# Kernel optimization log

Hardware: AMD Instinct MI355X
Metric: run time of the kernel (lower is better)

Reference implementation:

```python
import jax, jax.numpy as jnp
import numpy as np

N_NODES = 50000
IN_DIM = 5000
OUT_DIM = 128
NNZ_X = 1000000
NNZ_ADJ = 1600000


def setup_inputs() -> dict:
    key = jax.random.key(0)
    k1, k2, k3, k4, k5, k6, k7 = jax.random.split(key, 7)
    x_rows = jax.random.randint(k1, (NNZ_X,), 0, N_NODES, dtype=jnp.int32)
    x_cols = jax.random.randint(k2, (NNZ_X,), 0, IN_DIM, dtype=jnp.int32)
    x_vals = jax.random.normal(k3, (NNZ_X,), dtype=jnp.float32)
    adj_rows = jax.random.randint(k4, (NNZ_ADJ,), 0, N_NODES, dtype=jnp.int32)
    adj_cols = jax.random.randint(k5, (NNZ_ADJ,), 0, N_NODES, dtype=jnp.int32)
    adj_vals = jax.random.uniform(k6, (NNZ_ADJ,), dtype=jnp.float32)
    # Glorot-uniform init as in weight_variable_glorot
    init_range = np.sqrt(6.0 / (IN_DIM + OUT_DIM))
    W = jax.random.uniform(k7, (IN_DIM, OUT_DIM), dtype=jnp.float32,
                           minval=-init_range, maxval=init_range)
    return {"x_rows": x_rows, "x_cols": x_cols, "x_vals": x_vals,
            "adj_rows": adj_rows, "adj_cols": adj_cols, "adj_vals": adj_vals,
            "W": W}


def reference(x_rows, x_cols, x_vals, adj_rows, adj_cols, adj_vals, W):
    # dropout = 0 -> sparse dropout is identity (keep_prob = 1).
    # Step 1: xw = sparse_x @ W  -> [N, D] via gather rows of W + segment sum over node ids
    xw = jax.ops.segment_sum(x_vals[:, None] * W[x_cols], x_rows,
                             num_segments=N_NODES)  # [N, D]
    # Step 2: out = sparse_adj @ xw  -> gather neighbor features, weight, scatter-add
    agg = jax.ops.segment_sum(adj_vals[:, None] * xw[adj_cols], adj_rows,
                              num_segments=N_NODES)  # [N, D]
    return jax.nn.relu(agg)
```

## Files before the change

kernel.cpp:

```cpp
#include <hip/hip_runtime.h>

#define ODIM 128
#define BROWS 128
#define NBMAX 512
#define TILE 4096
#define CMASK 0x1FFFFu
#define HISTB 1024
#define CONVB 512

typedef unsigned u32;
typedef unsigned long long u64;

__device__ inline unsigned f2bf(float x) {
  unsigned u = __float_as_uint(x);
  return (u + 0x7fffu + ((u >> 16) & 1u)) >> 16;
}


__global__ __launch_bounds__(256) void hist_conv(
    const int* __restrict__ xr, int nx, const int* __restrict__ ar, int na,
    int* __restrict__ ghX, int* __restrict__ ghA,
    const float2* __restrict__ W2, u32* __restrict__ Wbf, int wwords) {
  __shared__ int lh[2 * NBMAX];
  if ((int)blockIdx.x >= HISTB) {
    int i = (blockIdx.x - HISTB) * 256 + threadIdx.x;
    int stride = CONVB * 256;
    for (; i < wwords; i += stride) {
      float2 w = W2[i];
      Wbf[i] = f2bf(w.x) | (f2bf(w.y) << 16);
    }
    return;
  }
  for (int i = threadIdx.x; i < 2 * NBMAX; i += 256) lh[i] = 0;
  __syncthreads();
  int total = nx + na;
  for (int i = blockIdx.x * 256 + threadIdx.x; i < total; i += HISTB * 256) {
    if (i < nx) atomicAdd(&lh[xr[i] >> 7], 1);
    else        atomicAdd(&lh[NBMAX + (ar[i - nx] >> 7)], 1);
  }
  __syncthreads();
  for (int b = threadIdx.x; b < NBMAX; b += 256) {
    if (lh[b])         atomicAdd(&ghX[b], lh[b]);
    if (lh[NBMAX + b]) atomicAdd(&ghA[b], lh[NBMAX + b]);
  }
}


__global__ __launch_bounds__(NBMAX) void scan_buckets(
    int* __restrict__ ghX, int* __restrict__ baseX, int* __restrict__ curX,
    int* __restrict__ ghA, int* __restrict__ baseA, int* __restrict__ curA,
    int nb) {
  int* gh   = blockIdx.x ? ghA   : ghX;
  int* base = blockIdx.x ? baseA : baseX;
  int* cur  = blockIdx.x ? curA  : curX;
  __shared__ int s[NBMAX];
  int tid = threadIdx.x;
  int v = (tid < nb) ? gh[tid] : 0;
  s[tid] = v;
  __syncthreads();
  for (int off = 1; off < NBMAX; off <<= 1) {
    int t = (tid >= off) ? s[tid - off] : 0;
    __syncthreads();
    s[tid] += t;
    __syncthreads();
  }
  int excl = s[tid] - v;
  if (tid < nb) { base[tid] = excl; cur[tid] = excl; }
  if (tid == NBMAX - 1) base[nb] = s[tid];
}


__global__ __launch_bounds__(256) void partition_both(
    const int* __restrict__ xr, const int* __restrict__ xc,
    const float* __restrict__ xv, int nx, int ntX,
    int* __restrict__ curX, uint2* __restrict__ outX,
    const int* __restrict__ ar, const int* __restrict__ ac,
    const float* __restrict__ av, int na,
    int* __restrict__ curA, uint2* __restrict__ outA) {
  __shared__ uint2 pay[TILE];
  __shared__ unsigned short bkt[TILE];
  __shared__ unsigned short perm[TILE];
  __shared__ int hist[NBMAX];
  __shared__ int scn[NBMAX];
  __shared__ int cur[NBMAX];
  __shared__ int gbase[NBMAX];
  __shared__ int part[256];

  const int* rows; const int* cols; const float* vals;
  int nnz; int* gcur; uint2* outbuf; int tile;
  if ((int)blockIdx.x < ntX) {
    rows = xr; cols = xc; vals = xv; nnz = nx; gcur = curX; outbuf = outX;
    tile = blockIdx.x;
  } else {
    rows = ar; cols = ac; vals = av; nnz = na; gcur = curA; outbuf = outA;
    tile = blockIdx.x - ntX;
  }

  int tid = threadIdx.x;
  int tbase = tile * TILE;
  int cnt = nnz - tbase; if (cnt > TILE) cnt = TILE;

  for (int b = tid; b < NBMAX; b += 256) hist[b] = 0;
  __syncthreads();

  for (int j = tid; j < cnt; j += 256) {
    int r = rows[tbase + j];
    int c = cols[tbase + j];
    float v = vals[tbase + j];
    unsigned b = (unsigned)r >> 7;
    bkt[j] = (unsigned short)b;
    pay[j] = make_uint2(((unsigned)(r & 127) << 17) | (unsigned)c, __float_as_uint(v));
    atomicAdd(&hist[b], 1);
  }
  __syncthreads();

  int h0 = hist[2 * tid], h1 = hist[2 * tid + 1];
  int psum = h0 + h1;
  part[tid] = psum;
  __syncthreads();
  for (int off = 1; off < 256; off <<= 1) {
    int t = (tid >= off) ? part[tid - off] : 0;
    __syncthreads();
    part[tid] += t;
    __syncthreads();
  }
  int excl = part[tid] - psum;
  scn[2 * tid] = excl;     scn[2 * tid + 1] = excl + h0;
  cur[2 * tid] = excl;     cur[2 * tid + 1] = excl + h0;
  __syncthreads();

  for (int j = tid; j < cnt; j += 256) {
    int pos = atomicAdd(&cur[bkt[j]], 1);
    perm[pos] = (unsigned short)j;
  }
  for (int b = tid; b < NBMAX; b += 256) {
    int c = hist[b];
    if (c) gbase[b] = atomicAdd(&gcur[b], c);
  }
  __syncthreads();

  for (int p = tid; p < cnt; p += 256) {
    int j = perm[p];
    int b = bkt[j];
    outbuf[gbase[b] + (p - scn[b])] = pay[j];
  }
}


__global__ __launch_bounds__(256) void bucket_sort_both(
    int nbX,
    const int* __restrict__ baseX, const uint2* __restrict__ binX,
    uint2* __restrict__ boutX, int* __restrict__ rpX,
    const int* __restrict__ baseA, const uint2* __restrict__ binA,
    uint2* __restrict__ boutA, int* __restrict__ rpA, int N) {
  __shared__ int hist[BROWS], scn[BROWS], cur[BROWS];
  const int* base; const uint2* bufin; uint2* bufout; int* rowptr; int b;
  if ((int)blockIdx.x < nbX) {
    base = baseX; bufin = binX; bufout = boutX; rowptr = rpX; b = blockIdx.x;
  } else {
    base = baseA; bufin = binA; bufout = boutA; rowptr = rpA; b = blockIdx.x - nbX;
  }
  int tid = threadIdx.x;
  int e0 = base[b], ecnt = base[b + 1] - e0;

  if (tid < BROWS) hist[tid] = 0;
  __syncthreads();
  for (int j = tid; j < ecnt; j += 256)
    atomicAdd(&hist[bufin[e0 + j].x >> 17], 1);
  __syncthreads();

  int v = (tid < BROWS) ? hist[tid] : 0;
  if (tid < BROWS) scn[tid] = v;
  __syncthreads();
  for (int off = 1; off < BROWS; off <<= 1) {
    int t = (tid < BROWS && tid >= off) ? scn[tid - off] : 0;
    __syncthreads();
    if (tid < BROWS) scn[tid] += t;
    __syncthreads();
  }
  if (tid < BROWS) {
    int excl = scn[tid] - v;
    cur[tid] = excl;
    int node = b * BROWS + tid;
    if (node <= N) rowptr[node] = e0 + excl;
  }
  __syncthreads();

  for (int j = tid; j < ecnt; j += 256) {
    uint2 e = bufin[e0 + j];
    int pos = atomicAdd(&cur[e.x >> 17], 1);
    bufout[e0 + pos] = e;
  }
}


__global__ __launch_bounds__(256) void pull_x(
    const int* __restrict__ rowptr, const uint2* __restrict__ cv,
    const u32* __restrict__ Wbf, unsigned* __restrict__ xw, int nrows) {
  int lane = threadIdx.x & 63;
  int r = blockIdx.x * 4 + (threadIdx.x >> 6);
  if (r >= nrows) return;
  int e = rowptr[r], end = rowptr[r + 1];
  const u64* cv8 = (const u64*)cv;
  float acc0[8], acc1[8];
#pragma unroll
  for (int u = 0; u < 8; ++u) { acc0[u] = 0.f; acc1[u] = 0.f; }
  for (; e + 7 < end; e += 8) {
    u64 pk[8]; unsigned xg[8];
#pragma unroll
    for (int u = 0; u < 8; ++u) pk[u] = __builtin_nontemporal_load(cv8 + e + u);
#pragma unroll
    for (int u = 0; u < 8; ++u)
      xg[u] = Wbf[(size_t)((unsigned)pk[u] & CMASK) * 64 + lane];
#pragma unroll
    for (int u = 0; u < 8; ++u) {
      float v = __uint_as_float((unsigned)(pk[u] >> 32));
      acc0[u] += v * __uint_as_float(xg[u] << 16);
      acc1[u] += v * __uint_as_float(xg[u] & 0xffff0000u);
    }
  }
  for (; e < end; ++e) {
    u64 pk = __builtin_nontemporal_load(cv8 + e);
    unsigned ua = Wbf[(size_t)((unsigned)pk & CMASK) * 64 + lane];
    float va = __uint_as_float((unsigned)(pk >> 32));
    acc0[0] += va * __uint_as_float(ua << 16);
    acc1[0] += va * __uint_as_float(ua & 0xffff0000u);
  }
  float o0 = ((acc0[0] + acc0[1]) + (acc0[2] + acc0[3])) +
             ((acc0[4] + acc0[5]) + (acc0[6] + acc0[7]));
  float o1 = ((acc1[0] + acc1[1]) + (acc1[2] + acc1[3])) +
             ((acc1[4] + acc1[5]) + (acc1[6] + acc1[7]));
  xw[(size_t)r * 64 + lane] = f2bf(o0) | (f2bf(o1) << 16);
}

__global__ __launch_bounds__(256) void pull_a(
    const int* __restrict__ rowptr, const uint2* __restrict__ cv,
    const unsigned* __restrict__ xw, float2* __restrict__ out, int nrows) {
  int lane = threadIdx.x & 63;
  int r = blockIdx.x * 4 + (threadIdx.x >> 6);
  if (r >= nrows) return;
  int e = rowptr[r], end = rowptr[r + 1];
  const u64* cv8 = (const u64*)cv;
  float acc0[8], acc1[8];
#pragma unroll
  for (int u = 0; u < 8; ++u) { acc0[u] = 0.f; acc1[u] = 0.f; }
  for (; e + 7 < end; e += 8) {
    u64 pk[8]; unsigned xg[8];
#pragma unroll
    for (int u = 0; u < 8; ++u) pk[u] = __builtin_nontemporal_load(cv8 + e + u);
#pragma unroll
    for (int u = 0; u < 8; ++u)
      xg[u] = xw[(size_t)((unsigned)pk[u] & CMASK) * 64 + lane];
#pragma unroll
    for (int u = 0; u < 8; ++u) {
      float v = __uint_as_float((unsigned)(pk[u] >> 32));
      acc0[u] += v * __uint_as_float(xg[u] << 16);
      acc1[u] += v * __uint_as_float(xg[u] & 0xffff0000u);
    }
  }
  for (; e < end; ++e) {
    u64 pk = __builtin_nontemporal_load(cv8 + e);
    unsigned ua = xw[(size_t)((unsigned)pk & CMASK) * 64 + lane];
    float va = __uint_as_float((unsigned)(pk >> 32));
    acc0[0] += va * __uint_as_float(ua << 16);
    acc1[0] += va * __uint_as_float(ua & 0xffff0000u);
  }
  float o0 = ((acc0[0] + acc0[1]) + (acc0[2] + acc0[3])) +
             ((acc0[4] + acc0[5]) + (acc0[6] + acc0[7]));
  float o1 = ((acc1[0] + acc1[1]) + (acc1[2] + acc1[3])) +
             ((acc1[4] + acc1[5]) + (acc1[6] + acc1[7]));
  u64 ov = (u64)__float_as_uint(fmaxf(o0, 0.f)) |
           ((u64)__float_as_uint(fmaxf(o1, 0.f)) << 32);
  __builtin_nontemporal_store(ov, (u64*)(out + (size_t)r * 64 + lane));
}


__global__ __launch_bounds__(256) void spmm_scatter(
    const int* __restrict__ rows, const int* __restrict__ cols,
    const float* __restrict__ vals, const float* __restrict__ B,
    float* __restrict__ out, int nnz) {
  int e = blockIdx.x * 2 + (threadIdx.x >> 7);
  int d = threadIdx.x & (ODIM - 1);
  if (e >= nnz) return;
  atomicAdd(&out[(size_t)rows[e] * ODIM + d],
            vals[e] * B[(size_t)cols[e] * ODIM + d]);
}

__global__ __launch_bounds__(256) void relu_inplace(float* __restrict__ p, long n4) {
  long i = (long)blockIdx.x * blockDim.x + threadIdx.x;
  long stride = (long)gridDim.x * blockDim.x;
  float4* p4 = (float4*)p;
  for (long j = i; j < n4; j += stride) {
    float4 v = p4[j];
    v.x = fmaxf(v.x, 0.f); v.y = fmaxf(v.y, 0.f);
    v.z = fmaxf(v.z, 0.f); v.w = fmaxf(v.w, 0.f);
    p4[j] = v;
  }
}

extern "C" void kernel_launch(void* const* d_in, const int* in_sizes, int n_in,
                              void* d_out, int out_size, void* d_ws, size_t ws_size,
                              hipStream_t stream) {
  const int*   x_rows   = (const int*)d_in[0];
  const int*   x_cols   = (const int*)d_in[1];
  const float* x_vals   = (const float*)d_in[2];
  const int*   adj_rows = (const int*)d_in[3];
  const int*   adj_cols = (const int*)d_in[4];
  const float* adj_vals = (const float*)d_in[5];
  const float* W        = (const float*)d_in[6];

  const int nnz_x   = in_sizes[0];
  const int nnz_adj = in_sizes[3];
  const int wlen    = in_sizes[6];
  const int N       = out_size / ODIM;
  const int NB      = (N + BROWS - 1) / BROWS;
  const int ntX     = (nnz_x + TILE - 1) / TILE;
  const int ntA     = (nnz_adj + TILE - 1) / TILE;
  const int wwords  = wlen / 2;

  float* out = (float*)d_out;

  char* p = (char*)d_ws;
  int* ghX   = (int*)p;  p += NBMAX * sizeof(int);
  int* ghA   = (int*)p;  p += NBMAX * sizeof(int);
  int* baseX = (int*)p;  p += (NBMAX + 1) * sizeof(int);
  int* baseA = (int*)p;  p += (NBMAX + 1) * sizeof(int);
  int* curX  = (int*)p;  p += NBMAX * sizeof(int);
  int* curA  = (int*)p;  p += NBMAX * sizeof(int);
  int* rpX   = (int*)p;  p += (size_t)(N + 1) * sizeof(int);
  int* rpA   = (int*)p;  p += (size_t)(N + 1) * sizeof(int);
  p = (char*)(((uintptr_t)p + 255) & ~(uintptr_t)255);
  u32* Wbf   = (u32*)p;  p += (size_t)wwords * sizeof(u32);
  p = (char*)(((uintptr_t)p + 255) & ~(uintptr_t)255);
  char* bufs = p;

  const size_t xw_bytes = (size_t)N * 64 * sizeof(u32);

  {
    char* q = bufs;
    uint2* bufPX = (uint2*)q; q += (size_t)nnz_x * sizeof(uint2);
    uint2* bufPA = (uint2*)q; q += (size_t)nnz_adj * sizeof(uint2);
    uint2* bufSX = (uint2*)q; q += (size_t)nnz_x * sizeof(uint2);
    uint2* bufSA = (uint2*)q; q += (size_t)nnz_adj * sizeof(uint2);
    size_t need = (size_t)(q - (char*)d_ws);
    bool xw_fits = xw_bytes <= ((size_t)nnz_x + nnz_adj) * sizeof(uint2);
    if (ws_size >= need && NB <= NBMAX && xw_fits) {
      u32* xw = (u32*)bufPX;
      (void)hipMemsetAsync(ghX, 0, 2 * NBMAX * sizeof(int), stream);
      hist_conv<<<HISTB + CONVB, 256, 0, stream>>>(
          x_rows, nnz_x, adj_rows, nnz_adj, ghX, ghA,
          (const float2*)W, Wbf, wwords);
      scan_buckets<<<2, NBMAX, 0, stream>>>(ghX, baseX, curX, ghA, baseA, curA, NB);
      partition_both<<<ntX + ntA, 256, 0, stream>>>(
          x_rows, x_cols, x_vals, nnz_x, ntX, curX, bufPX,
          adj_rows, adj_cols, adj_vals, nnz_adj, curA, bufPA);
      bucket_sort_both<<<2 * NB, 256, 0, stream>>>(
          NB, baseX, bufPX, bufSX, rpX, baseA, bufPA, bufSA, rpA, N);
      pull_x<<<(N + 3) / 4, 256, 0, stream>>>(rpX, bufSX, Wbf, xw, N);
      pull_a<<<(N + 3) / 4, 256, 0, stream>>>(rpA, bufSA, xw, (float2*)out, N);
      return;
    }
  }

  {
    size_t bufP_elems = (size_t)(nnz_x > nnz_adj ? nnz_x : nnz_adj);
    if (bufP_elems * sizeof(uint2) < xw_bytes)
      bufP_elems = (xw_bytes + sizeof(uint2) - 1) / sizeof(uint2);
    char* q = bufs;
    uint2* bufP  = (uint2*)q; q += bufP_elems * sizeof(uint2);
    uint2* bufSX = (uint2*)q; q += (size_t)nnz_x * sizeof(uint2);
    uint2* bufSA = (uint2*)q; q += (size_t)nnz_adj * sizeof(uint2);
    size_t need = (size_t)(q - (char*)d_ws);
    if (ws_size >= need && NB <= NBMAX) {
      u32* xw = (u32*)bufP;
      (void)hipMemsetAsync(ghX, 0, 2 * NBMAX * sizeof(int), stream);
      hist_conv<<<HISTB + CONVB, 256, 0, stream>>>(
          x_rows, nnz_x, adj_rows, nnz_adj, ghX, ghA,
          (const float2*)W, Wbf, wwords);
      scan_buckets<<<2, NBMAX, 0, stream>>>(ghX, baseX, curX, ghA, baseA, curA, NB);
      partition_both<<<ntX, 256, 0, stream>>>(
          x_rows, x_cols, x_vals, nnz_x, ntX, curX, bufP,
          adj_rows, adj_cols, adj_vals, nnz_adj, curA, bufP);
      bucket_sort_both<<<NB, 256, 0, stream>>>(
          NB, baseX, bufP, bufSX, rpX, baseA, bufP, bufSA, rpA, N);
      partition_both<<<ntA, 256, 0, stream>>>(
          x_rows, x_cols, x_vals, nnz_x, 0, curX, bufP,
          adj_rows, adj_cols, adj_vals, nnz_adj, curA, bufP);
      bucket_sort_both<<<NB, 256, 0, stream>>>(
          0, baseX, bufP, bufSX, rpX, baseA, bufP, bufSA, rpA, N);
      pull_x<<<(N + 3) / 4, 256, 0, stream>>>(rpX, bufSX, Wbf, xw, N);
      pull_a<<<(N + 3) / 4, 256, 0, stream>>>(rpA, bufSA, xw, (float2*)out, N);
      return;
    }
  }

  {
    float* xwf = (float*)d_ws;
    const size_t out_bytes = (size_t)out_size * sizeof(float);
    (void)hipMemsetAsync(xwf, 0, out_bytes, stream);
    (void)hipMemsetAsync(out, 0, out_bytes, stream);
    spmm_scatter<<<(nnz_x + 1) / 2, 256, 0, stream>>>(x_rows, x_cols, x_vals, W, xwf, nnz_x);
    spmm_scatter<<<(nnz_adj + 1) / 2, 256, 0, stream>>>(adj_rows, adj_cols, adj_vals, xwf, out, nnz_adj);
    relu_inplace<<<2048, 256, 0, stream>>>(out, (long)out_size / 4);
  }
}
```

Before: 198.6 us.

## Fuse per-bucket row sort with SpMM pull into one LDS-staged kernel

Replaces the separate bucket_sort and pull_x/pull_a kernels with a templated kernel that loads each 128-row bucket's edges into shared memory in chunks, counting-sorts them by local row via a permutation array, and has each wave accumulate 16 rows directly from LDS. This removes the global write and re-read of the sorted edge arrays and the rowptr arrays, and drops one launch per stage. The cost is far fewer blocks (one per bucket, about 391) with large LDS use. Each wave handles 16 rows sequentially with 32 accumulators, which lowers parallelism and occupancy for the gather-bound pull.

```diff
diff --git a/kernel.cpp b/kernel.cpp
--- a/kernel.cpp
+++ b/kernel.cpp
@@ -4,6 +4,7 @@
 #define BROWS 128
 #define NBMAX 512
 #define TILE 4096
+#define CH 4608
 #define CMASK 0x1FFFFu
 #define HISTB 1024
 #define CONVB 512
@@ -147,131 +148,100 @@
 }
 
 
-__global__ __launch_bounds__(256) void bucket_sort_both(
-    int nbX,
-    const int* __restrict__ baseX, const uint2* __restrict__ binX,
-    uint2* __restrict__ boutX, int* __restrict__ rpX,
-    const int* __restrict__ baseA, const uint2* __restrict__ binA,
-    uint2* __restrict__ boutA, int* __restrict__ rpA, int N) {
-  __shared__ int hist[BROWS], scn[BROWS], cur[BROWS];
-  const int* base; const uint2* bufin; uint2* bufout; int* rowptr; int b;
-  if ((int)blockIdx.x < nbX) {
-    base = baseX; bufin = binX; bufout = boutX; rowptr = rpX; b = blockIdx.x;
-  } else {
-    base = baseA; bufin = binA; bufout = boutA; rowptr = rpA; b = blockIdx.x - nbX;
-  }
+template <bool ISX>
+__global__ __launch_bounds__(512) void fused_sort_pull(
+    const int* __restrict__ base, const uint2* __restrict__ bufP,
+    const u32* __restrict__ table,
+    u32* __restrict__ xwout,
+    float2* __restrict__ aout,
+    int N) {
+  __shared__ uint2 pay[CH];
+  __shared__ unsigned short perm[CH];
+  __shared__ int hist[BROWS], startb[BROWS], cur[BROWS];
   int tid = threadIdx.x;
-  int e0 = base[b], ecnt = base[b + 1] - e0;
-
-  if (tid < BROWS) hist[tid] = 0;
-  __syncthreads();
-  for (int j = tid; j < ecnt; j += 256)
-    atomicAdd(&hist[bufin[e0 + j].x >> 17], 1);
-  __syncthreads();
-
-  int v = (tid < BROWS) ? hist[tid] : 0;
-  if (tid < BROWS) scn[tid] = v;
-  __syncthreads();
-  for (int off = 1; off < BROWS; off <<= 1) {
-    int t = (tid < BROWS && tid >= off) ? scn[tid - off] : 0;
-    __syncthreads();
-    if (tid < BROWS) scn[tid] += t;
-    __syncthreads();
-  }
-  if (tid < BROWS) {
-    int excl = scn[tid] - v;
-    cur[tid] = excl;
-    int node = b * BROWS + tid;
-    if (node <= N) rowptr[node] = e0 + excl;
-  }
-  __syncthreads();
-
-  for (int j = tid; j < ecnt; j += 256) {
-    uint2 e = bufin[e0 + j];
-    int pos = atomicAdd(&cur[e.x >> 17], 1);
-    bufout[e0 + pos] = e;
-  }
-}
-
-
-__global__ __launch_bounds__(256) void pull_x(
-    const int* __restrict__ rowptr, const uint2* __restrict__ cv,
-    const u32* __restrict__ Wbf, unsigned* __restrict__ xw, int nrows) {
-  int lane = threadIdx.x & 63;
-  int r = blockIdx.x * 4 + (threadIdx.x >> 6);
-  if (r >= nrows) return;
-  int e = rowptr[r], end = rowptr[r + 1];
-  const u64* cv8 = (const u64*)cv;
-  float acc0[8], acc1[8];
-#pragma unroll
-  for (int u = 0; u < 8; ++u) { acc0[u] = 0.f; acc1[u] = 0.f; }
-  for (; e + 7 < end; e += 8) {
-    u64 pk[8]; unsigned xg[8];
-#pragma unroll
-    for (int u = 0; u < 8; ++u) pk[u] = __builtin_nontemporal_load(cv8 + e + u);
-#pragma unroll
-    for (int u = 0; u < 8; ++u)
-      xg[u] = Wbf[(size_t)((unsigned)pk[u] & CMASK) * 64 + lane];
-#pragma unroll
-    for (int u = 0; u < 8; ++u) {
-      float v = __uint_as_float((unsigned)(pk[u] >> 32));
-      acc0[u] += v * __uint_as_float(xg[u] << 16);
-      acc1[u] += v * __uint_as_float(xg[u] & 0xffff0000u);
-    }
-  }
-  for (; e < end; ++e) {
-    u64 pk = __builtin_nontemporal_load(cv8 + e);
-    unsigned ua = Wbf[(size_t)((unsigned)pk & CMASK) * 64 + lane];
-    float va = __uint_as_float((unsigned)(pk >> 32));
-    acc0[0] += va * __uint_as_float(ua << 16);
-    acc1[0] += va * __uint_as_float(ua & 0xffff0000u);
-  }
-  float o0 = ((acc0[0] + acc0[1]) + (acc0[2] + acc0[3])) +
-             ((acc0[4] + acc0[5]) + (acc0[6] + acc0[7]));
-  float o1 = ((acc1[0] + acc1[1]) + (acc1[2] + acc1[3])) +
-             ((acc1[4] + acc1[5]) + (acc1[6] + acc1[7]));
-  xw[(size_t)r * 64 + lane] = f2bf(o0) | (f2bf(o1) << 16);
-}
-
-__global__ __launch_bounds__(256) void pull_a(
-    const int* __restrict__ rowptr, const uint2* __restrict__ cv,
-    const unsigned* __restrict__ xw, float2* __restrict__ out, int nrows) {
-  int lane = threadIdx.x & 63;
-  int r = blockIdx.x * 4 + (threadIdx.x >> 6);
-  if (r >= nrows) return;
-  int e = rowptr[r], end = rowptr[r + 1];
-  const u64* cv8 = (const u64*)cv;
-  float acc0[8], acc1[8];
-#pragma unroll
-  for (int u = 0; u < 8; ++u) { acc0[u] = 0.f; acc1[u] = 0.f; }
-  for (; e + 7 < end; e += 8) {
-    u64 pk[8]; unsigned xg[8];
-#pragma unroll
-    for (int u = 0; u < 8; ++u) pk[u] = __builtin_nontemporal_load(cv8 + e + u);
-#pragma unroll
-    for (int u = 0; u < 8; ++u)
-      xg[u] = xw[(size_t)((unsigned)pk[u] & CMASK) * 64 + lane];
-#pragma unroll
-    for (int u = 0; u < 8; ++u) {
-      float v = __uint_as_float((unsigned)(pk[u] >> 32));
-      acc0[u] += v * __uint_as_float(xg[u] << 16);
-      acc1[u] += v * __uint_as_float(xg[u] & 0xffff0000u);
-    }
-  }
-  for (; e < end; ++e) {
-    u64 pk = __builtin_nontemporal_load(cv8 + e);
-    unsigned ua = xw[(size_t)((unsigned)pk & CMASK) * 64 + lane];
-    float va = __uint_as_float((unsigned)(pk >> 32));
-    acc0[0] += va * __uint_as_float(ua << 16);
-    acc1[0] += va * __uint_as_float(ua & 0xffff0000u);
-  }
-  float o0 = ((acc0[0] + acc0[1]) + (acc0[2] + acc0[3])) +
-             ((acc0[4] + acc0[5]) + (acc0[6] + acc0[7]));
-  float o1 = ((acc1[0] + acc1[1]) + (acc1[2] + acc1[3])) +
-             ((acc1[4] + acc1[5]) + (acc1[6] + acc1[7]));
-  u64 ov = (u64)__float_as_uint(fmaxf(o0, 0.f)) |
-           ((u64)__float_as_uint(fmaxf(o1, 0.f)) << 32);
-  __builtin_nontemporal_store(ov, (u64*)(out + (size_t)r * 64 + lane));
+  int lane = tid & 63;
+  int w = tid >> 6;
+  int b = blockIdx.x;
+  int e0 = base[b], etot = base[b + 1] - e0;
+
+  float acc0[16], acc1[16];
+#pragma unroll
+  for (int i = 0; i < 16; ++i) { acc0[i] = 0.f; acc1[i] = 0.f; }
+
+  for (int coff = 0; coff < etot; coff += CH) {
+    int cnt = etot - coff; if (cnt > CH) cnt = CH;
+    __syncthreads();
+    if (tid < BROWS) hist[tid] = 0;
+    __syncthreads();
+    for (int j = tid; j < cnt; j += 512) {
+      uint2 e = bufP[e0 + coff + j];
+      pay[j] = e;
+      atomicAdd(&hist[e.x >> 17], 1);
+    }
+    __syncthreads();
+    int v = (tid < BROWS) ? hist[tid] : 0;
+    if (tid < BROWS) startb[tid] = v;
+    __syncthreads();
+    for (int off = 1; off < BROWS; off <<= 1) {
+      int t = (tid < BROWS && tid >= off) ? startb[tid - off] : 0;
+      __syncthreads();
+      if (tid < BROWS) startb[tid] += t;
+      __syncthreads();
+    }
+    if (tid < BROWS) {
+      int excl = startb[tid] - v;
+      startb[tid] = excl;
+      cur[tid] = excl;
+    }
+    __syncthreads();
+    for (int j = tid; j < cnt; j += 512) {
+      int pos = atomicAdd(&cur[pay[j].x >> 17], 1);
+      perm[pos] = (unsigned short)j;
+    }
+    __syncthreads();
+#pragma unroll
+    for (int rr = 0; rr < 16; ++rr) {
+      int r = w * 16 + rr;
+      int e = startb[r];
+      int eend = e + hist[r];
+      for (; e + 7 < eend; e += 8) {
+        unsigned mt[8]; float vv[8]; unsigned xg[8];
+#pragma unroll
+        for (int u = 0; u < 8; ++u) {
+          uint2 t = pay[perm[e + u]];
+          mt[u] = t.x; vv[u] = __uint_as_float(t.y);
+        }
+#pragma unroll
+        for (int u = 0; u < 8; ++u)
+          xg[u] = table[(size_t)(mt[u] & CMASK) * 64 + lane];
+#pragma unroll
+        for (int u = 0; u < 8; ++u) {
+          acc0[rr] += vv[u] * __uint_as_float(xg[u] << 16);
+          acc1[rr] += vv[u] * __uint_as_float(xg[u] & 0xffff0000u);
+        }
+      }
+      for (; e < eend; ++e) {
+        uint2 t = pay[perm[e]];
+        unsigned ua = table[(size_t)(t.x & CMASK) * 64 + lane];
+        float va = __uint_as_float(t.y);
+        acc0[rr] += va * __uint_as_float(ua << 16);
+        acc1[rr] += va * __uint_as_float(ua & 0xffff0000u);
+      }
+    }
+  }
+
+#pragma unroll
+  for (int rr = 0; rr < 16; ++rr) {
+    int node = b * BROWS + w * 16 + rr;
+    if (node < N) {
+      if (ISX) {
+        xwout[(size_t)node * 64 + lane] = f2bf(acc0[rr]) | (f2bf(acc1[rr]) << 16);
+      } else {
+        aout[(size_t)node * 64 + lane] =
+            make_float2(fmaxf(acc0[rr], 0.f), fmaxf(acc1[rr], 0.f));
+      }
+    }
+  }
 }
 
 
@@ -327,71 +297,27 @@
   int* baseA = (int*)p;  p += (NBMAX + 1) * sizeof(int);
   int* curX  = (int*)p;  p += NBMAX * sizeof(int);
   int* curA  = (int*)p;  p += NBMAX * sizeof(int);
-  int* rpX   = (int*)p;  p += (size_t)(N + 1) * sizeof(int);
-  int* rpA   = (int*)p;  p += (size_t)(N + 1) * sizeof(int);
   p = (char*)(((uintptr_t)p + 255) & ~(uintptr_t)255);
   u32* Wbf   = (u32*)p;  p += (size_t)wwords * sizeof(u32);
   p = (char*)(((uintptr_t)p + 255) & ~(uintptr_t)255);
-  char* bufs = p;
-
-  const size_t xw_bytes = (size_t)N * 64 * sizeof(u32);
-
-  {
-    char* q = bufs;
-    uint2* bufPX = (uint2*)q; q += (size_t)nnz_x * sizeof(uint2);
-    uint2* bufPA = (uint2*)q; q += (size_t)nnz_adj * sizeof(uint2);
-    uint2* bufSX = (uint2*)q; q += (size_t)nnz_x * sizeof(uint2);
-    uint2* bufSA = (uint2*)q; q += (size_t)nnz_adj * sizeof(uint2);
-    size_t need = (size_t)(q - (char*)d_ws);
-    bool xw_fits = xw_bytes <= ((size_t)nnz_x + nnz_adj) * sizeof(uint2);
-    if (ws_size >= need && NB <= NBMAX && xw_fits) {
-      u32* xw = (u32*)bufPX;
-      (void)hipMemsetAsync(ghX, 0, 2 * NBMAX * sizeof(int), stream);
-      hist_conv<<<HISTB + CONVB, 256, 0, stream>>>(
-          x_rows, nnz_x, adj_rows, nnz_adj, ghX, ghA,
-          (const float2*)W, Wbf, wwords);
-      scan_buckets<<<2, NBMAX, 0, stream>>>(ghX, baseX, curX, ghA, baseA, curA, NB);
-      partition_both<<<ntX + ntA, 256, 0, stream>>>(
-          x_rows, x_cols, x_vals, nnz_x, ntX, curX, bufPX,
-          adj_rows, adj_cols, adj_vals, nnz_adj, curA, bufPA);
-      bucket_sort_both<<<2 * NB, 256, 0, stream>>>(
-          NB, baseX, bufPX, bufSX, rpX, baseA, bufPA, bufSA, rpA, N);
-      pull_x<<<(N + 3) / 4, 256, 0, stream>>>(rpX, bufSX, Wbf, xw, N);
-      pull_a<<<(N + 3) / 4, 256, 0, stream>>>(rpA, bufSA, xw, (float2*)out, N);
-      return;
-    }
-  }
-
-  {
-    size_t bufP_elems = (size_t)(nnz_x > nnz_adj ? nnz_x : nnz_adj);
-    if (bufP_elems * sizeof(uint2) < xw_bytes)
-      bufP_elems = (xw_bytes + sizeof(uint2) - 1) / sizeof(uint2);
-    char* q = bufs;
-    uint2* bufP  = (uint2*)q; q += bufP_elems * sizeof(uint2);
-    uint2* bufSX = (uint2*)q; q += (size_t)nnz_x * sizeof(uint2);
-    uint2* bufSA = (uint2*)q; q += (size_t)nnz_adj * sizeof(uint2);
-    size_t need = (size_t)(q - (char*)d_ws);
-    if (ws_size >= need && NB <= NBMAX) {
-      u32* xw = (u32*)bufP;
-      (void)hipMemsetAsync(ghX, 0, 2 * NBMAX * sizeof(int), stream);
-      hist_conv<<<HISTB + CONVB, 256, 0, stream>>>(
-          x_rows, nnz_x, adj_rows, nnz_adj, ghX, ghA,
-          (const float2*)W, Wbf, wwords);
-      scan_buckets<<<2, NBMAX, 0, stream>>>(ghX, baseX, curX, ghA, baseA, curA, NB);
-      partition_both<<<ntX, 256, 0, stream>>>(
-          x_rows, x_cols, x_vals, nnz_x, ntX, curX, bufP,
-          adj_rows, adj_cols, adj_vals, nnz_adj, curA, bufP);
-      bucket_sort_both<<<NB, 256, 0, stream>>>(
-          NB, baseX, bufP, bufSX, rpX, baseA, bufP, bufSA, rpA, N);
-      partition_both<<<ntA, 256, 0, stream>>>(
-          x_rows, x_cols, x_vals, nnz_x, 0, curX, bufP,
-          adj_rows, adj_cols, adj_vals, nnz_adj, curA, bufP);
-      bucket_sort_both<<<NB, 256, 0, stream>>>(
-          0, baseX, bufP, bufSX, rpX, baseA, bufP, bufSA, rpA, N);
-      pull_x<<<(N + 3) / 4, 256, 0, stream>>>(rpX, bufSX, Wbf, xw, N);
-      pull_a<<<(N + 3) / 4, 256, 0, stream>>>(rpA, bufSA, xw, (float2*)out, N);
-      return;
-    }
+  u32* xw    = (u32*)p;  p += (size_t)N * 64 * sizeof(u32);
+  p = (char*)(((uintptr_t)p + 255) & ~(uintptr_t)255);
+  uint2* bufPX = (uint2*)p; p += (size_t)nnz_x * sizeof(uint2);
+  uint2* bufPA = (uint2*)p; p += (size_t)nnz_adj * sizeof(uint2);
+  size_t need = (size_t)(p - (char*)d_ws);
+
+  if (ws_size >= need && NB <= NBMAX) {
+    (void)hipMemsetAsync(ghX, 0, 2 * NBMAX * sizeof(int), stream);
+    hist_conv<<<HISTB + CONVB, 256, 0, stream>>>(
+        x_rows, nnz_x, adj_rows, nnz_adj, ghX, ghA,
+        (const float2*)W, Wbf, wwords);
+    scan_buckets<<<2, NBMAX, 0, stream>>>(ghX, baseX, curX, ghA, baseA, curA, NB);
+    partition_both<<<ntX + ntA, 256, 0, stream>>>(
+        x_rows, x_cols, x_vals, nnz_x, ntX, curX, bufPX,
+        adj_rows, adj_cols, adj_vals, nnz_adj, curA, bufPA);
+    fused_sort_pull<true><<<NB, 512, 0, stream>>>(baseX, bufPX, Wbf, xw, nullptr, N);
+    fused_sort_pull<false><<<NB, 512, 0, stream>>>(baseA, bufPA, xw, nullptr, (float2*)out, N);
+    return;
   }
 
   {
```

After: 185.1 us. 1.07x faster.
